# Performance work log

Measured on AMD Instinct MI355X. Metric: run time of the kernel, lower is better.

## Reference

```python
import jax, jax.numpy as jnp
import numpy as np


def conv2d(x, w, b, pad):
    # x: [B,Cin,H,W], w: [Cout,Cin,kh,kw]
    y = jax.lax.conv_general_dilated(
        x, w, window_strides=(1, 1), padding=[(pad, pad), (pad, pad)],
        dimension_numbers=('NCHW', 'OIHW', 'NCHW'))
    return y + b[None, :, None, None]


def setup_inputs() -> dict:
    key = jax.random.key(0)
    ks = jax.random.split(key, 11)
    B, C, H, W = 4, 128, 64, 64
    Cc, Hc, Wc = 256, 32, 32
    s = 0.05
    return {
        'sr_feat': jax.random.normal(ks[0], (B, C, H, W), jnp.float32),
        'context_feat': jax.random.normal(ks[1], (B, Cc, Hc, Wc), jnp.float32),
        'Wq': jax.random.normal(ks[2], (C, C, 1, 1), jnp.float32) * s,
        'bq': jax.random.normal(ks[3], (C,), jnp.float32) * s,
        'Wk': jax.random.normal(ks[4], (C, Cc, 1, 1), jnp.float32) * s,
        'bk': jax.random.normal(ks[5], (C,), jnp.float32) * s,
        'Wv': jax.random.normal(ks[6], (C, Cc, 1, 1), jnp.float32) * s,
        'bv': jax.random.normal(ks[7], (C,), jnp.float32) * s,
        'Wp': jax.random.normal(ks[8], (C, C, 3, 3), jnp.float32) * s,
        'bp': jax.random.normal(ks[9], (C,), jnp.float32) * s,
        'gamma': jax.random.normal(ks[10], (1,), jnp.float32) * s,
    }


def reference(sr_feat, context_feat, Wq, bq, Wk, bk, Wv, bv, Wp, bp, gamma):
    B, C, H, W = sr_feat.shape
    Cc = context_feat.shape[1]
    # bilinear upsample (half-pixel centers == align_corners=False)
    ctx = jax.image.resize(context_feat, (B, Cc, H, W), method='bilinear')
    q = conv2d(sr_feat, Wq, bq, 0).reshape(B, C, H * W)   # [B,C,N]
    k = conv2d(ctx, Wk, bk, 0).reshape(B, C, H * W)       # [B,C,N]
    v = conv2d(ctx, Wv, bv, 0).reshape(B, C, H * W)       # [B,C,N]
    # attn[b,n,m] = softmax_m( sum_c q[b,c,n] * k[b,c,m] )
    attn = jax.nn.softmax(jnp.einsum('bcn,bcm->bnm', q, k), axis=-1)
    # out[b,c,n] = sum_m v[b,c,m] * attn[b,n,m]
    out = jnp.einsum('bcm,bnm->bcn', v, attn).reshape(B, C, H, W)
    return sr_feat + gamma[0] * conv2d(out, Wp, bp, 1)
```

## Files before the change

kernel.cpp:

```cpp
#include <hip/hip_runtime.h>
#include <math.h>

#define NB 4
#define C  128
#define CCH 256
#define HH 64
#define WW 64
#define NN 4096
#define NS 1024
#define HC 32
#define WC 32
#define PP 66
#define LOG2E 1.44269504088896f
#define NSPLIT 4

typedef unsigned short u16;
typedef unsigned int uint32;
typedef short s16x8 __attribute__((ext_vector_type(8)));
typedef float f32x4 __attribute__((ext_vector_type(4)));
typedef float f32x16 __attribute__((ext_vector_type(16)));

#if __has_builtin(__builtin_amdgcn_exp2f)
#define EXP2(x) __builtin_amdgcn_exp2f(x)
#else
#define EXP2(x) __expf((x) * 0.69314718056f)
#endif

__device__ __forceinline__ u16 f2bf(float f) {
    uint32 u = __float_as_uint(f);
    u += 0x7fffu + ((u >> 16) & 1u);
    return (u16)(u >> 16);
}
__device__ __forceinline__ float bf2f(u16 h) {
    return __uint_as_float((uint32)h << 16);
}

__global__ __launch_bounds__(256) void prep2(const float* __restrict__ ctx,
                                             const float* __restrict__ sr,
                                             const float* __restrict__ Wq,
                                             const float* __restrict__ Wk,
                                             const float* __restrict__ Wv,
                                             const float* __restrict__ Wp,
                                             u16* __restrict__ ctx_s,
                                             u16* __restrict__ sr_t,
                                             u16* __restrict__ wbf,
                                             u16* __restrict__ wt,
                                             uint4* __restrict__ att_z) {
    __shared__ float ls[64 * 65];
    int blk = blockIdx.x;
    int tid = threadIdx.x;

    if (blk < 256) {
        int idx = blk;
        int n0 = (idx & 15) * 64;
        int ci0 = ((idx >> 4) & 3) * 64;
        int b = idx >> 6;
        const float* inb = ctx + ((size_t)b * CCH + ci0) * NS + n0;
#pragma unroll
        for (int L = 0; L < 4; L++) {
            int fc = tid + L * 256;
            int nc = fc & 15, ci = fc >> 4;
            float4 v = *(const float4*)(inb + (size_t)ci * NS + nc * 4);
            float* d = &ls[ci * 65 + nc * 4];
            d[0] = v.x; d[1] = v.y; d[2] = v.z; d[3] = v.w;
        }
        __syncthreads();
        u16* ob = ctx_s + ((size_t)b * NS + n0) * CCH + ci0;
#pragma unroll
        for (int j = 0; j < 16; j++) {
            int o = tid + j * 256;
            int ci = o & 63, n = o >> 6;
            ob[(size_t)n * CCH + ci] = f2bf(ls[ci * 65 + n]);
        }
    } else if (blk < 768) {
        int idx = blk - 256;
        int n0 = (idx & 63) * 64;
        int ci0 = ((idx >> 6) & 1) * 64;
        int b = idx >> 7;
        const float* inb = sr + ((size_t)b * C + ci0) * NN + n0;
#pragma unroll
        for (int L = 0; L < 4; L++) {
            int fc = tid + L * 256;
            int nc = fc & 15, ci = fc >> 4;
            float4 v = *(const float4*)(inb + (size_t)ci * NN + nc * 4);
            float* d = &ls[ci * 65 + nc * 4];
            d[0] = v.x; d[1] = v.y; d[2] = v.z; d[3] = v.w;
        }
        __syncthreads();
        u16* ob = sr_t + ((size_t)b * NN + n0) * C + ci0;
#pragma unroll
        for (int j = 0; j < 16; j++) {
            int o = tid + j * 256;
            int ci = o & 63, n = o >> 6;
            ob[(size_t)n * C + ci] = f2bf(ls[ci * 65 + n]);
        }
    } else if (blk < 1664) {
        int i = (blk - 768) * 256 + tid;
        if (i < 81920) {
            float v;
            if (i < 16384) v = Wq[i] * LOG2E;
            else if (i < 49152) v = Wk[i - 16384];
            else v = Wv[i - 49152];
            wbf[i] = f2bf(v);
        } else {
            int idx = i - 81920;
            int ciin = idx & 31;
            int co = (idx >> 5) & 127;
            int cb = (idx >> 12) & 3;
            int pos = idx >> 14;
            int ky = pos / 3, kx = pos - ky * 3;
            int ci = cb * 32 + ciin;
            wt[idx] = f2bf(Wp[((size_t)(co * C + ci) * 3 + ky) * 3 + kx]);
        }
    } else {
        int i = (blk - 1664) * 256 + tid;
        if (i < 278784) att_z[i] = make_uint4(0, 0, 0, 0);
    }
}

__global__ __launch_bounds__(256) void proj_all2(const u16* __restrict__ sr_t,
                                                 const u16* __restrict__ ctx_s,
                                                 const u16* __restrict__ wbf,
                                                 const float* __restrict__ bq,
                                                 const float* __restrict__ bk,
                                                 const float* __restrict__ bv,
                                                 u16* __restrict__ q_t,
                                                 u16* __restrict__ k_s,
                                                 u16* __restrict__ v_s) {
    __shared__ u16 xs[128 * 64];
    __shared__ u16 wsm[2][128 * 64];
    int b = blockIdx.y;
    int tid = threadIdx.x;
    int w = tid >> 6, lane = tid & 63, l31 = lane & 31, half = lane >> 5;
    int xh = w >> 1, wh = w & 1;

    if (blockIdx.x < 32) {
        int n0 = blockIdx.x * 128;
        const u16* xb = sr_t + (size_t)b * NN * C;
        f32x16 acc[2][2];
#pragma unroll
        for (int xt = 0; xt < 2; xt++)
#pragma unroll
            for (int wt2 = 0; wt2 < 2; wt2++)
#pragma unroll
                for (int i = 0; i < 16; i++) acc[xt][wt2][i] = 0.f;
        for (int c0i = 0; c0i < 2; c0i++) {
            int c0 = c0i * 64;
            __syncthreads();
#pragma unroll
            for (int t = 0; t < 4; t++) {
                int CI = t * 256 + tid;
                int row = CI >> 3, sl = CI & 7;
                int lc = sl ^ (row & 7);
                __builtin_amdgcn_global_load_lds(
                    (const __attribute__((address_space(1))) void*)(xb + (size_t)(n0 + row) * C + c0 + lc * 8),
                    (__attribute__((address_space(3))) void*)&xs[(size_t)CI * 8], 16, 0, 0);
            }
#pragma unroll
            for (int t = 0; t < 4; t++) {
                int CI = t * 256 + tid;
                int co = CI >> 3, sl = CI & 7;
                int lc = sl ^ (co & 7);
                __builtin_amdgcn_global_load_lds(
                    (const __attribute__((address_space(1))) void*)(wbf + (size_t)co * C + c0 + lc * 8),
                    (__attribute__((address_space(3))) void*)&wsm[0][(size_t)CI * 8], 16, 0, 0);
            }
            __syncthreads();
#pragma unroll
            for (int kg = 0; kg < 4; kg++) {
                int pc = ((kg * 2 + half) ^ (l31 & 7)) * 8;
                s16x8 xf[2], wf2[2];
#pragma unroll
                for (int xt = 0; xt < 2; xt++)
                    xf[xt] = *(const s16x8*)&xs[(xh * 64 + xt * 32 + l31) * 64 + pc];
#pragma unroll
                for (int wt2 = 0; wt2 < 2; wt2++)
                    wf2[wt2] = *(const s16x8*)&wsm[0][(wh * 64 + wt2 * 32 + l31) * 64 + pc];
#pragma unroll
                for (int xt = 0; xt < 2; xt++)
#pragma unroll
                    for (int wt2 = 0; wt2 < 2; wt2++)
                        acc[xt][wt2] = __builtin_amdgcn_mfma_f32_32x32x16_bf16(xf[xt], wf2[wt2], acc[xt][wt2], 0, 0, 0);
            }
        }
        u16* ot = q_t + (size_t)b * NN * C;
        float bv2[2];
#pragma unroll
        for (int wt2 = 0; wt2 < 2; wt2++) bv2[wt2] = bq[wh * 64 + wt2 * 32 + l31] * LOG2E;
#pragma unroll
        for (int xt = 0; xt < 2; xt++)
#pragma unroll
            for (int r = 0; r < 16; r++) {
                int n = n0 + xh * 64 + xt * 32 + (r & 3) + 8 * (r >> 2) + 4 * half;
#pragma unroll
                for (int wt2 = 0; wt2 < 2; wt2++)
                    ot[(size_t)n * C + wh * 64 + wt2 * 32 + l31] = f2bf(acc[xt][wt2][r] + bv2[wt2]);
            }
    } else {
        int n0 = (blockIdx.x - 32) * 64;
        const u16* xb = ctx_s + (size_t)b * NS * CCH;
        const u16* wkb = wbf + 16384;
        const u16* wvb = wbf + 49152;
        f32x16 acck[2], accv[2];
#pragma unroll
        for (int wt2 = 0; wt2 < 2; wt2++)
#pragma unroll
            for (int i = 0; i < 16; i++) { acck[wt2][i] = 0.f; accv[wt2][i] = 0.f; }
        for (int c0i = 0; c0i < 4; c0i++) {
            int c0 = c0i * 64;
            __syncthreads();
#pragma unroll
            for (int t = 0; t < 2; t++) {
                int CI = t * 256 + tid;
                int row = CI >> 3, sl = CI & 7;
                int lc = sl ^ (row & 7);
                __builtin_amdgcn_global_load_lds(
                    (const __attribute__((address_space(1))) void*)(xb + (size_t)(n0 + row) * CCH + c0 + lc * 8),
                    (__attribute__((address_space(3))) void*)&xs[(size_t)CI * 8], 16, 0, 0);
            }
#pragma unroll
            for (int t = 0; t < 4; t++) {
                int CI = t * 256 + tid;
                int co = CI >> 3, sl = CI & 7;
                int lc = sl ^ (co & 7);
                __builtin_amdgcn_global_load_lds(
                    (const __attribute__((address_space(1))) void*)(wkb + (size_t)co * CCH + c0 + lc * 8),
                    (__attribute__((address_space(3))) void*)&wsm[0][(size_t)CI * 8], 16, 0, 0);
            }
#pragma unroll
            for (int t = 0; t < 4; t++) {
                int CI = t * 256 + tid;
                int co = CI >> 3, sl = CI & 7;
                int lc = sl ^ (co & 7);
                __builtin_amdgcn_global_load_lds(
                    (const __attribute__((address_space(1))) void*)(wvb + (size_t)co * CCH + c0 + lc * 8),
                    (__attribute__((address_space(3))) void*)&wsm[1][(size_t)CI * 8], 16, 0, 0);
            }
            __syncthreads();
#pragma unroll
            for (int kg = 0; kg < 4; kg++) {
                int pc = ((kg * 2 + half) ^ (l31 & 7)) * 8;
                s16x8 xf = *(const s16x8*)&xs[(xh * 32 + l31) * 64 + pc];
                s16x8 wfk[2], wfv[2];
#pragma unroll
                for (int wt2 = 0; wt2 < 2; wt2++) {
                    wfk[wt2] = *(const s16x8*)&wsm[0][(wh * 64 + wt2 * 32 + l31) * 64 + pc];
                    wfv[wt2] = *(const s16x8*)&wsm[1][(wh * 64 + wt2 * 32 + l31) * 64 + pc];
                }
#pragma unroll
                for (int wt2 = 0; wt2 < 2; wt2++) {
                    acck[wt2] = __builtin_amdgcn_mfma_f32_32x32x16_bf16(xf, wfk[wt2], acck[wt2], 0, 0, 0);
                    accv[wt2] = __builtin_amdgcn_mfma_f32_32x32x16_bf16(wfv[wt2], xf, accv[wt2], 0, 0, 0);
                }
            }
        }
        u16* ok = k_s + (size_t)b * NS * C;
#pragma unroll
        for (int wt2 = 0; wt2 < 2; wt2++) {
            float bvk = bk[wh * 64 + wt2 * 32 + l31];
#pragma unroll
            for (int r = 0; r < 16; r++) {
                int n = n0 + xh * 32 + (r & 3) + 8 * (r >> 2) + 4 * half;
                ok[(size_t)n * C + wh * 64 + wt2 * 32 + l31] = f2bf(acck[wt2][r] + bvk);
            }
        }
        u16* ov = v_s + (size_t)b * C * NS;
#pragma unroll
        for (int wt2 = 0; wt2 < 2; wt2++)
#pragma unroll
            for (int r = 0; r < 16; r++) {
                int co = wh * 64 + wt2 * 32 + (r & 3) + 8 * (r >> 2) + 4 * half;
                ov[(size_t)co * NS + n0 + xh * 32 + l31] = f2bf(accv[wt2][r] + bv[co]);
            }
    }
}

__global__ __launch_bounds__(256) void upsample_v(const u16* __restrict__ v_s,
                                                  u16* __restrict__ v_bf) {
    __shared__ u16 lsv[NS];
    int idx = blockIdx.x;
    int tid = threadIdx.x;
    int c = idx & 127, b = idx >> 7;
    const u16* vp = v_s + ((size_t)b * C + c) * NS;
    if (tid < 128) *(uint4*)&lsv[tid * 8] = *(const uint4*)(vp + tid * 8);
    __syncthreads();
    u16* ob = v_bf + ((size_t)b * C + c) * NN;
#pragma unroll
    for (int j = 0; j < 16; j++) {
        int n = tid + j * 256;
        int y = n >> 6, x = n & 63;
        float sy = y * 0.5f - 0.25f;
        float sx = x * 0.5f - 0.25f;
        int y0 = (int)floorf(sy), x0 = (int)floorf(sx);
        float wy = sy - (float)y0, wx = sx - (float)x0;
        int y0c = y0 < 0 ? 0 : y0;
        int y1c = (y0 + 1 > HC - 1) ? HC - 1 : y0 + 1;
        int x0c = x0 < 0 ? 0 : x0;
        int x1c = (x0 + 1 > WC - 1) ? WC - 1 : x0 + 1;
        float v00 = bf2f(lsv[y0c * WC + x0c]), v01 = bf2f(lsv[y0c * WC + x1c]);
        float v10 = bf2f(lsv[y1c * WC + x0c]), v11 = bf2f(lsv[y1c * WC + x1c]);
        ob[n] = f2bf((1.f - wy) * ((1.f - wx) * v00 + wx * v01)
                   +        wy  * ((1.f - wx) * v10 + wx * v11));
    }
}

__global__ __launch_bounds__(256, 2) void flash_mfma(const u16* __restrict__ qt_p,
                                                     const u16* __restrict__ ks_p,
                                                     const u16* __restrict__ vt_p,
                                                     u16* __restrict__ part,
                                                     float* __restrict__ lpart) {
    __shared__ u16 ksr[3][32 * 128];
    __shared__ u16 vs[2][128 * 64];

    int ib = blockIdx.x;
    int b = (ib & 7) >> 1;
    int rest = ((ib >> 3) << 1) | (ib & 1);
    int qtile = rest >> 2;
    int split = rest & 3;
    int n0 = qtile * 128;
    int tid = threadIdx.x;
    int w = tid >> 6, lane = tid & 63, l31 = lane & 31, half = lane >> 5;

    const u16* qtb = qt_p + (size_t)b * NN * C;
    const u16* ksb = ks_p + (size_t)b * NS * C;
    const u16* vtb = vt_p + (size_t)b * C * NN;

    auto stageKrow = [&](int buf, int r) {
#pragma unroll
        for (int t = 0; t < 2; t++) {
            int CI = t * 256 + tid;
            int row = CI >> 4;
            int lc = (CI & 15) ^ (row & 15);
            __builtin_amdgcn_global_load_lds(
                (const __attribute__((address_space(1))) void*)(ksb + (size_t)(r * 32 + row) * C + lc * 8),
                (__attribute__((address_space(3))) void*)&ksr[buf][(size_t)CI * 8], 16, 0, 0);
        }
    };
    auto stageV = [&](int buf, int m0) {
#pragma unroll
        for (int t = 0; t < 4; t++) {
            int CI = (w * 4 + t) * 64 + lane;
            int c = CI >> 3;
            int lc = (CI & 7) ^ (c & 7);
            __builtin_amdgcn_global_load_lds(
                (const __attribute__((address_space(1))) void*)(vtb + (size_t)c * NN + m0 + lc * 8),
                (__attribute__((address_space(3))) void*)&vs[buf][(w * 4 + t) * 512], 16, 0, 0);
        }
    };

    int qrow = n0 + w * 32 + l31;
    s16x8 qf[8];
#pragma unroll
    for (int kg = 0; kg < 8; kg++)
        qf[kg] = *(const s16x8*)(qtb + (size_t)qrow * C + kg * 16 + half * 8);

    auto scoreTile = [&](int buf) {
        f32x16 st;
#pragma unroll
        for (int i = 0; i < 16; i++) st[i] = 0.f;
        const u16* kb = &ksr[buf][0];
#pragma unroll
        for (int kg = 0; kg < 8; kg++) {
            int pc = ((kg * 2 + half) ^ (l31 & 15)) * 8;
            s16x8 kf = *(const s16x8*)&kb[l31 * 128 + pc];
            st = __builtin_amdgcn_mfma_f32_32x32x16_bf16(kf, qf[kg], st, 0, 0, 0);
        }
        return st;
    };

    int m_base = split * 1024;
    int j0 = split * 8;

    stageKrow(0, split == 0 ? 0 : j0 - 1);
    stageKrow(1, j0);
    stageKrow(2, j0 + 1);
    stageV(0, m_base);
    __syncthreads();
    f32x16 sA = scoreTile(0);
    f32x16 sB = scoreTile(1);
    f32x16 sC;

    f32x16 oacc[4];
#pragma unroll
    for (int mt = 0; mt < 4; mt++)
#pragma unroll
        for (int i = 0; i < 16; i++) oacc[mt][i] = 0.f;
    float lsum = 0.f;

#pragma unroll 2
    for (int it = 0; it < 16; it++) {
        int buf = it & 1;
        int m0 = m_base + it * 64;
        if (it < 15) {
            stageV(buf ^ 1, m0 + 64);
            if (it & 1) {
                int rs = j0 + 2 + (it >> 1);
                if (rs <= 31) stageKrow((it >> 1) % 3, rs);
            }
        }
        if (!(it & 1)) {
            int rn = j0 + 1 + (it >> 1);
            if (rn <= 31) sC = scoreTile((2 + (it >> 1)) % 3);
        } else {
            sA = sB;
            int rn = j0 + 1 + (it >> 1);
            if (rn <= 31) sB = sC;
        }

        float wB = (it & 1) ? 0.25f : 0.75f;
        float wA = 1.0f - wB;
        float cc[16];
#pragma unroll
        for (int i = 0; i < 16; i++) cc[i] = wA * sA[i] + wB * sB[i];

        float xr0  = __shfl_xor(cc[0], 32);
        float xr3  = __shfl_xor(cc[3], 32);
        float xr4  = __shfl_xor(cc[4], 32);
        float xr7  = __shfl_xor(cc[7], 32);
        float xr8  = __shfl_xor(cc[8], 32);
        float xr11 = __shfl_xor(cc[11], 32);
        float xr12 = __shfl_xor(cc[12], 32);
        float xr15 = __shfl_xor(cc[15], 32);
        float d0s[4], d5s[4];
        d0s[0] = half ? xr3  : cc[0];
        d0s[1] = half ? xr7  : xr3;
        d0s[2] = half ? xr11 : xr7;
        d0s[3] = half ? xr15 : xr11;
        d5s[0] = half ? xr4  : xr0;
        d5s[1] = half ? xr8  : xr4;
        d5s[2] = half ? xr12 : xr8;
        d5s[3] = half ? cc[15] : xr12;

        const u16* vsb = &vs[buf][0];
#pragma unroll
        for (int s = 0; s < 4; s++) {
            float d0 = d0s[s], d1 = cc[4 * s], d2 = cc[4 * s + 1];
            float d3 = cc[4 * s + 2], d4 = cc[4 * s + 3], d5 = d5s[s];
            float e1 = 0.75f * d1, e2 = 0.75f * d2, e3 = 0.75f * d3, e4 = 0.75f * d4;
            float p0 = EXP2(fmaf(0.25f, d0, e1));
            float p1 = EXP2(fmaf(0.25f, d2, e1));
            float p2 = EXP2(fmaf(0.25f, d1, e2));
            float p3 = EXP2(fmaf(0.25f, d3, e2));
            float p4 = EXP2(fmaf(0.25f, d2, e3));
            float p5 = EXP2(fmaf(0.25f, d4, e3));
            float p6 = EXP2(fmaf(0.25f, d3, e4));
            float p7 = EXP2(fmaf(0.25f, d5, e4));
            lsum += ((p0 + p1) + (p2 + p3)) + ((p4 + p5) + (p6 + p7));
            union { uint32 u[4]; s16x8 v; } pu;
            pu.u[0] = __builtin_amdgcn_perm(__float_as_uint(p1), __float_as_uint(p0), 0x07060302u);
            pu.u[1] = __builtin_amdgcn_perm(__float_as_uint(p3), __float_as_uint(p2), 0x07060302u);
            pu.u[2] = __builtin_amdgcn_perm(__float_as_uint(p5), __float_as_uint(p4), 0x07060302u);
            pu.u[3] = __builtin_amdgcn_perm(__float_as_uint(p7), __float_as_uint(p6), 0x07060302u);
            int pcv = ((s * 2 + half) ^ (l31 & 7)) * 8;
#pragma unroll
            for (int mt = 0; mt < 4; mt++) {
                s16x8 vf = *(const s16x8*)&vsb[(mt * 32 + l31) * 64 + pcv];
                oacc[mt] = __builtin_amdgcn_mfma_f32_32x32x16_bf16(vf, pu.v, oacc[mt], 0, 0, 0);
            }
        }
        __syncthreads();
    }

    float lt = lsum + __shfl_xor(lsum, 32);
    if (half == 0) lpart[(size_t)split * NB * NN + (size_t)b * NN + qrow] = lt;
    u16* pb = part + ((size_t)split * NB + b) * (size_t)C * NN;
#pragma unroll
    for (int mt = 0; mt < 4; mt++)
#pragma unroll
        for (int r = 0; r < 16; r++) {
            int c = mt * 32 + (r & 3) + 8 * (r >> 2) + 4 * half;
            pb[(size_t)c * NN + n0 + w * 32 + l31] = f2bf(oacc[mt][r]);
        }
}

__global__ __launch_bounds__(256) void flash_combine(const u16* __restrict__ part,
                                                     const float* __restrict__ lpart,
                                                     u16* __restrict__ att_t) {
    __shared__ u16 ts[128 * 66];
    __shared__ float linv[64];
    int b = blockIdx.y;
    int nt = blockIdx.x;
    int n0 = nt * 64;
    int tid = threadIdx.x;
    if (tid < 64) {
        float s = 0.f;
#pragma unroll
        for (int sp = 0; sp < NSPLIT; sp++)
            s += lpart[(size_t)sp * NB * NN + (size_t)b * NN + n0 + tid];
        linv[tid] = 1.0f / s;
    }
    __syncthreads();
#pragma unroll
    for (int j = 0; j < 32; j++) {
        int e = tid + j * 256;
        int n = e & 63, c = e >> 6;
        float o = 0.f;
#pragma unroll
        for (int sp = 0; sp < NSPLIT; sp++)
            o += bf2f(part[((size_t)sp * NB + b) * (size_t)C * NN + (size_t)c * NN + n0 + n]);
        ts[c * 66 + n] = f2bf(o * linv[n]);
    }
    __syncthreads();
    u16* ob = att_t + ((size_t)b * PP * PP + (size_t)(nt + 1) * PP + 1) * C;
#pragma unroll
    for (int j = 0; j < 32; j++) {
        int o = tid + j * 256;
        int c = o & 127, n = o >> 7;
        ob[(size_t)n * C + c] = ts[c * 66 + n];
    }
}

__global__ __launch_bounds__(256) void conv3x3_mfma(const u16* __restrict__ att_t,
                                                    const u16* __restrict__ wt,
                                                    const float* __restrict__ bp,
                                                    const float* __restrict__ sr,
                                                    const float* __restrict__ gamma,
                                                    float* __restrict__ out) {
    __shared__ u16 in_s[2][4 * 102 * 8];
    int ib = blockIdx.x;
    int b = (ib & 7) >> 1;
    int rr = ((ib >> 3) << 1) | (ib & 1);
    int y = rr >> 1;
    int x0 = (rr & 1) * 32;
    int tid = threadIdx.x;
    int w = tid >> 6, lane = tid & 63, l = tid & 15, quad = (tid >> 4) & 3;
    const u16* ab = att_t + (size_t)b * (PP * PP * C);

    auto stage = [&](int cib, int bufi) {
        u16* base = &in_s[bufi][w * 102 * 8];
        const u16* gsrc = ab + cib * 32 + w * 8;
#pragma unroll
        for (int t = 0; t < 2; t++) {
            int idx = t * 64 + lane;
            int r = idx / 34, xp = idx - r * 34;
            if (t == 0 || lane < 38)
                __builtin_amdgcn_global_load_lds(
                    (const __attribute__((address_space(1))) void*)(gsrc + (size_t)((y + r) * PP + x0 + xp) * C),
                    (__attribute__((address_space(3))) void*)(base + (size_t)t * 64 * 8), 16, 0, 0);
        }
    };

    f32x4 accr[2][2];
#pragma unroll
    for (int cf = 0; cf < 2; cf++)
#pragma unroll
        for (int nf = 0; nf < 2; nf++) accr[cf][nf] = (f32x4){0.f, 0.f, 0.f, 0.f};
    int cow = w * 32;

    stage(0, 0);
    __syncthreads();
#pragma unroll
    for (int cib = 0; cib < 4; cib++) {
        if (cib < 3) stage(cib + 1, (cib + 1) & 1);
        s16x8 wf[9][2];
#pragma unroll
        for (int pos = 0; pos < 9; pos++)
#pragma unroll
            for (int cf = 0; cf < 2; cf++)
                wf[pos][cf] = *(const s16x8*)&wt[((size_t)(pos * 4 + cib) * C + cow + cf * 16 + l) * 32 + quad * 8];
        const u16* bufc = &in_s[cib & 1][0];
#pragma unroll
        for (int ky = 0; ky < 3; ky++)
#pragma unroll
            for (int kx = 0; kx < 3; kx++) {
                int pos = ky * 3 + kx;
#pragma unroll
                for (int nf = 0; nf < 2; nf++) {
                    s16x8 inf = *(const s16x8*)&bufc[(quad * 102 + ky * 34 + nf * 16 + l + kx) * 8];
                    accr[0][nf] = __builtin_amdgcn_mfma_f32_16x16x32_bf16(wf[pos][0], inf, accr[0][nf], 0, 0, 0);
                    accr[1][nf] = __builtin_amdgcn_mfma_f32_16x16x32_bf16(wf[pos][1], inf, accr[1][nf], 0, 0, 0);
                }
            }
        __syncthreads();
    }

    float g = gamma[0];
    float* ob = out + (size_t)b * C * NN;
    const float* sb = sr + (size_t)b * C * NN;
#pragma unroll
    for (int cf = 0; cf < 2; cf++)
#pragma unroll
        for (int r = 0; r < 4; r++) {
            int co = cow + cf * 16 + quad * 4 + r;
            float bias = bp[co];
#pragma unroll
            for (int nf = 0; nf < 2; nf++) {
                size_t oo = (size_t)co * NN + y * 64 + x0 + nf * 16 + l;
                ob[oo] = sb[oo] + g * (accr[cf][nf][r] + bias);
            }
        }
}

extern "C" void kernel_launch(void* const* d_in, const int* in_sizes, int n_in,
                              void* d_out, int out_size, void* d_ws, size_t ws_size,
                              hipStream_t stream) {
    const float* sr    = (const float*)d_in[0];
    const float* ctx   = (const float*)d_in[1];
    const float* Wq    = (const float*)d_in[2];
    const float* bq    = (const float*)d_in[3];
    const float* Wk    = (const float*)d_in[4];
    const float* bk    = (const float*)d_in[5];
    const float* Wv    = (const float*)d_in[6];
    const float* bv    = (const float*)d_in[7];
    const float* Wp    = (const float*)d_in[8];
    const float* bp    = (const float*)d_in[9];
    const float* gamma = (const float*)d_in[10];
    float* out = (float*)d_out;

    char* wsb = (char*)d_ws;
    u16*   att_t  = (u16*)wsb;
    u16*   part   = (u16*)(wsb + (5u << 20));
    float* lpart  = (float*)(wsb + (21u << 20));
    u16*   ctx_s  = (u16*)(wsb + (22u << 20));
    u16*   sr_t   = (u16*)(wsb + (25u << 20));
    u16*   q_t    = (u16*)(wsb + (29u << 20));
    u16*   k_s    = (u16*)(wsb + (33u << 20));
    u16*   v_s    = (u16*)(wsb + (34u << 20));
    u16*   v_bf   = (u16*)(wsb + (39u << 20));
    u16*   wt     = (u16*)(wsb + (43u << 20));
    u16*   w_bf   = (u16*)(wsb + (43u << 20) + (512u << 10));

    prep2<<<dim3(2753), 256, 0, stream>>>(ctx, sr, Wq, Wk, Wv, Wp,
                                          ctx_s, sr_t, w_bf, wt, (uint4*)att_t);
    proj_all2<<<dim3(48, NB), 256, 0, stream>>>(sr_t, ctx_s, w_bf, bq, bk, bv,
                                                q_t, k_s, v_s);
    upsample_v<<<dim3(512), 256, 0, stream>>>(v_s, v_bf);
    flash_mfma<<<dim3(512), 256, 0, stream>>>(q_t, k_s, v_bf, part, lpart);
    flash_combine<<<dim3(64, NB), 256, 0, stream>>>(part, lpart, att_t);
    conv3x3_mfma<<<dim3(512), 256, 0, stream>>>(att_t, wt, bp, sr, gamma, out);
}
```

Baseline: 150.2 us.

## Fold V upsampling into attention weights and drop upsample_v kernel

Bilinear upsampling is linear, so attention against the upsampled V equals attention against low-resolution V with the probability rows folded by the transposed interpolation weights. The flash kernel now accumulates the folded probabilities per coarse row into two rotating accumulators and runs P·V against the 32x32 V directly. This removes the upsample_v launch, the full-resolution V buffer and its LDS staging, and cuts the P·V MFMA work. In exchange V fragments are read straight from global memory without LDS, there is extra VALU and shuffle work to fold the probabilities, and the edge-weight handling at split boundaries is subtle.

```diff
diff --git a/kernel.cpp b/kernel.cpp
--- a/kernel.cpp
+++ b/kernel.cpp
@@ -275,42 +275,12 @@
     }
 }
 
-__global__ __launch_bounds__(256) void upsample_v(const u16* __restrict__ v_s,
-                                                  u16* __restrict__ v_bf) {
-    __shared__ u16 lsv[NS];
-    int idx = blockIdx.x;
-    int tid = threadIdx.x;
-    int c = idx & 127, b = idx >> 7;
-    const u16* vp = v_s + ((size_t)b * C + c) * NS;
-    if (tid < 128) *(uint4*)&lsv[tid * 8] = *(const uint4*)(vp + tid * 8);
-    __syncthreads();
-    u16* ob = v_bf + ((size_t)b * C + c) * NN;
-#pragma unroll
-    for (int j = 0; j < 16; j++) {
-        int n = tid + j * 256;
-        int y = n >> 6, x = n & 63;
-        float sy = y * 0.5f - 0.25f;
-        float sx = x * 0.5f - 0.25f;
-        int y0 = (int)floorf(sy), x0 = (int)floorf(sx);
-        float wy = sy - (float)y0, wx = sx - (float)x0;
-        int y0c = y0 < 0 ? 0 : y0;
-        int y1c = (y0 + 1 > HC - 1) ? HC - 1 : y0 + 1;
-        int x0c = x0 < 0 ? 0 : x0;
-        int x1c = (x0 + 1 > WC - 1) ? WC - 1 : x0 + 1;
-        float v00 = bf2f(lsv[y0c * WC + x0c]), v01 = bf2f(lsv[y0c * WC + x1c]);
-        float v10 = bf2f(lsv[y1c * WC + x0c]), v11 = bf2f(lsv[y1c * WC + x1c]);
-        ob[n] = f2bf((1.f - wy) * ((1.f - wx) * v00 + wx * v01)
-                   +        wy  * ((1.f - wx) * v10 + wx * v11));
-    }
-}
-
 __global__ __launch_bounds__(256, 2) void flash_mfma(const u16* __restrict__ qt_p,
                                                      const u16* __restrict__ ks_p,
-                                                     const u16* __restrict__ vt_p,
+                                                     const u16* __restrict__ vs_p,
                                                      u16* __restrict__ part,
                                                      float* __restrict__ lpart) {
     __shared__ u16 ksr[3][32 * 128];
-    __shared__ u16 vs[2][128 * 64];
 
     int ib = blockIdx.x;
     int b = (ib & 7) >> 1;
@@ -323,7 +293,7 @@
 
     const u16* qtb = qt_p + (size_t)b * NN * C;
     const u16* ksb = ks_p + (size_t)b * NS * C;
-    const u16* vtb = vt_p + (size_t)b * C * NN;
+    const u16* vtb = vs_p + (size_t)b * C * NS;
 
     auto stageKrow = [&](int buf, int r) {
 #pragma unroll
@@ -336,17 +306,6 @@
                 (__attribute__((address_space(3))) void*)&ksr[buf][(size_t)CI * 8], 16, 0, 0);
         }
     };
-    auto stageV = [&](int buf, int m0) {
-#pragma unroll
-        for (int t = 0; t < 4; t++) {
-            int CI = (w * 4 + t) * 64 + lane;
-            int c = CI >> 3;
-            int lc = (CI & 7) ^ (c & 7);
-            __builtin_amdgcn_global_load_lds(
-                (const __attribute__((address_space(1))) void*)(vtb + (size_t)c * NN + m0 + lc * 8),
-                (__attribute__((address_space(3))) void*)&vs[buf][(w * 4 + t) * 512], 16, 0, 0);
-        }
-    };
 
     int qrow = n0 + w * 32 + l31;
     s16x8 qf[8];
@@ -368,13 +327,11 @@
         return st;
     };
 
-    int m_base = split * 1024;
     int j0 = split * 8;
 
     stageKrow(0, split == 0 ? 0 : j0 - 1);
     stageKrow(1, j0);
     stageKrow(2, j0 + 1);
-    stageV(0, m_base);
     __syncthreads();
     f32x16 sA = scoreTile(0);
     f32x16 sB = scoreTile(1);
@@ -385,34 +342,45 @@
     for (int mt = 0; mt < 4; mt++)
 #pragma unroll
         for (int i = 0; i < 16; i++) oacc[mt][i] = 0.f;
+    f32x16 acc0, acc1;
+#pragma unroll
+    for (int i = 0; i < 16; i++) { acc0[i] = 0.f; acc1[i] = 0.f; }
     float lsum = 0.f;
 
-#pragma unroll 2
-    for (int it = 0; it < 16; it++) {
-        int buf = it & 1;
-        int m0 = m_base + it * 64;
-        if (it < 15) {
-            stageV(buf ^ 1, m0 + 64);
-            if (it & 1) {
-                int rs = j0 + 2 + (it >> 1);
-                if (rs <= 31) stageKrow((it >> 1) % 3, rs);
-            }
-        }
-        if (!(it & 1)) {
-            int rn = j0 + 1 + (it >> 1);
-            if (rn <= 31) sC = scoreTile((2 + (it >> 1)) % 3);
-        } else {
-            sA = sB;
-            int rn = j0 + 1 + (it >> 1);
-            if (rn <= 31) sB = sC;
-        }
-
-        float wB = (it & 1) ? 0.25f : 0.75f;
-        float wA = 1.0f - wB;
-        float cc[16];
+    auto doPV = [&](int r, f32x16& ac) {
+        uint32 own[8], rcv[8];
+#pragma unroll
+        for (int s = 0; s < 4; s++) {
+            own[2 * s]     = __builtin_amdgcn_perm(__float_as_uint(ac[4 * s + 1]), __float_as_uint(ac[4 * s + 0]), 0x07060302u);
+            own[2 * s + 1] = __builtin_amdgcn_perm(__float_as_uint(ac[4 * s + 3]), __float_as_uint(ac[4 * s + 2]), 0x07060302u);
+        }
+#pragma unroll
+        for (int i = 0; i < 8; i++) rcv[i] = __shfl_xor(own[i], 32);
+        union { uint32 u[4]; s16x8 v; } pf0, pf1;
+        pf0.u[0] = half ? rcv[2] : own[0];
+        pf0.u[1] = half ? rcv[3] : own[1];
+        pf0.u[2] = half ? own[2] : rcv[0];
+        pf0.u[3] = half ? own[3] : rcv[1];
+        pf1.u[0] = half ? rcv[6] : own[4];
+        pf1.u[1] = half ? rcv[7] : own[5];
+        pf1.u[2] = half ? own[6] : rcv[4];
+        pf1.u[3] = half ? own[7] : rcv[5];
+        const u16* vr = vtb + (size_t)l31 * NS + (size_t)r * 32 + half * 8;
+#pragma unroll
+        for (int mt = 0; mt < 4; mt++) {
+            s16x8 vf0 = *(const s16x8*)(vr + (size_t)mt * 32 * NS);
+            s16x8 vf1 = *(const s16x8*)(vr + (size_t)mt * 32 * NS + 16);
+            oacc[mt] = __builtin_amdgcn_mfma_f32_32x32x16_bf16(vf0, pf0.v, oacc[mt], 0, 0, 0);
+            oacc[mt] = __builtin_amdgcn_mfma_f32_32x32x16_bf16(vf1, pf1.v, oacc[mt], 0, 0, 0);
+        }
+#pragma unroll
+        for (int i = 0; i < 16; i++) ac[i] = 0.f;
+    };
+
+    auto process = [&](float wA, float wB, float wlo, float whi, f32x16& alo, f32x16& ahi) {
+        f32x16 cc;
 #pragma unroll
         for (int i = 0; i < 16; i++) cc[i] = wA * sA[i] + wB * sB[i];
-
         float xr0  = __shfl_xor(cc[0], 32);
         float xr3  = __shfl_xor(cc[3], 32);
         float xr4  = __shfl_xor(cc[4], 32);
@@ -431,35 +399,85 @@
         d5s[2] = half ? xr12 : xr8;
         d5s[3] = half ? cc[15] : xr12;
 
-        const u16* vsb = &vs[buf][0];
+        float ps[4][8];
+        float r0a[4], r7a[4];
 #pragma unroll
         for (int s = 0; s < 4; s++) {
             float d0 = d0s[s], d1 = cc[4 * s], d2 = cc[4 * s + 1];
             float d3 = cc[4 * s + 2], d4 = cc[4 * s + 3], d5 = d5s[s];
             float e1 = 0.75f * d1, e2 = 0.75f * d2, e3 = 0.75f * d3, e4 = 0.75f * d4;
-            float p0 = EXP2(fmaf(0.25f, d0, e1));
-            float p1 = EXP2(fmaf(0.25f, d2, e1));
-            float p2 = EXP2(fmaf(0.25f, d1, e2));
-            float p3 = EXP2(fmaf(0.25f, d3, e2));
-            float p4 = EXP2(fmaf(0.25f, d2, e3));
-            float p5 = EXP2(fmaf(0.25f, d4, e3));
-            float p6 = EXP2(fmaf(0.25f, d3, e4));
-            float p7 = EXP2(fmaf(0.25f, d5, e4));
-            lsum += ((p0 + p1) + (p2 + p3)) + ((p4 + p5) + (p6 + p7));
-            union { uint32 u[4]; s16x8 v; } pu;
-            pu.u[0] = __builtin_amdgcn_perm(__float_as_uint(p1), __float_as_uint(p0), 0x07060302u);
-            pu.u[1] = __builtin_amdgcn_perm(__float_as_uint(p3), __float_as_uint(p2), 0x07060302u);
-            pu.u[2] = __builtin_amdgcn_perm(__float_as_uint(p5), __float_as_uint(p4), 0x07060302u);
-            pu.u[3] = __builtin_amdgcn_perm(__float_as_uint(p7), __float_as_uint(p6), 0x07060302u);
-            int pcv = ((s * 2 + half) ^ (l31 & 7)) * 8;
-#pragma unroll
-            for (int mt = 0; mt < 4; mt++) {
-                s16x8 vf = *(const s16x8*)&vsb[(mt * 32 + l31) * 64 + pcv];
-                oacc[mt] = __builtin_amdgcn_mfma_f32_32x32x16_bf16(vf, pu.v, oacc[mt], 0, 0, 0);
-            }
-        }
-        __syncthreads();
+            ps[s][0] = EXP2(fmaf(0.25f, d0, e1));
+            ps[s][1] = EXP2(fmaf(0.25f, d2, e1));
+            ps[s][2] = EXP2(fmaf(0.25f, d1, e2));
+            ps[s][3] = EXP2(fmaf(0.25f, d3, e2));
+            ps[s][4] = EXP2(fmaf(0.25f, d2, e3));
+            ps[s][5] = EXP2(fmaf(0.25f, d4, e3));
+            ps[s][6] = EXP2(fmaf(0.25f, d3, e4));
+            ps[s][7] = EXP2(fmaf(0.25f, d5, e4));
+            r0a[s] = __shfl_xor(ps[s][0], 32);
+            r7a[s] = __shfl_xor(ps[s][7], 32);
+        }
+        float tq[16];
+#pragma unroll
+        for (int s = 0; s < 4; s++) {
+            float pl = half ? r7a[s] : (s ? r7a[s - 1] : ps[0][0]);
+            float pr = half ? (s < 3 ? r0a[s + 1] : ps[3][7]) : r0a[s];
+            tq[4 * s + 0] = fmaf(0.25f, pl,       fmaf(0.75f, ps[s][0], fmaf(0.75f, ps[s][1], 0.25f * ps[s][2])));
+            tq[4 * s + 1] = fmaf(0.25f, ps[s][1], fmaf(0.75f, ps[s][2], fmaf(0.75f, ps[s][3], 0.25f * ps[s][4])));
+            tq[4 * s + 2] = fmaf(0.25f, ps[s][3], fmaf(0.75f, ps[s][4], fmaf(0.75f, ps[s][5], 0.25f * ps[s][6])));
+            tq[4 * s + 3] = fmaf(0.25f, ps[s][5], fmaf(0.75f, ps[s][6], fmaf(0.75f, ps[s][7], 0.25f * pr)));
+        }
+        float l0 = ((tq[0] + tq[1]) + (tq[2] + tq[3])) + ((tq[4] + tq[5]) + (tq[6] + tq[7]));
+        float l1 = ((tq[8] + tq[9]) + (tq[10] + tq[11])) + ((tq[12] + tq[13]) + (tq[14] + tq[15]));
+        lsum += l0 + l1;
+#pragma unroll
+        for (int i = 0; i < 16; i++) {
+            alo[i] = fmaf(wlo, tq[i], alo[i]);
+            ahi[i] = fmaf(whi, tq[i], ahi[i]);
+        }
+    };
+
+    float w0lo = (split == 0) ? 0.f : 0.25f;
+    float w0hi = (split == 0) ? 1.f : 0.75f;
+    float w15lo = (split == 3) ? 1.f : 0.75f;
+    float w15hi = (split == 3) ? 0.f : 0.25f;
+
+#pragma unroll
+    for (int it = 0; it < 16; it++) {
+        if ((it & 1) == 0) {
+            int rn = j0 + 1 + (it >> 1);
+            if (rn <= 31) sC = scoreTile((2 + (it >> 1)) % 3);
+            float wlo = (it == 0) ? w0lo : 0.25f;
+            float whi = (it == 0) ? w0hi : 0.75f;
+            f32x16& alo = (((it >> 1) & 1) == 0) ? acc0 : acc1;
+            f32x16& ahi = (((it >> 1) & 1) == 0) ? acc1 : acc0;
+            process(0.25f, 0.75f, wlo, whi, alo, ahi);
+            if (it != 0) {
+                doPV(j0 + (it >> 1) - 1, alo);
+            } else if (split != 0) {
+                doPV(j0 - 1, alo);
+            }
+            if (it == 0) __syncthreads();
+        } else {
+            if (it < 15) {
+                int rs = j0 + 2 + (it >> 1);
+                if (rs <= 31) stageKrow((it >> 1) % 3, rs);
+            }
+            sA = sB;
+            {
+                int rn = j0 + 1 + (it >> 1);
+                if (rn <= 31) sB = sC;
+            }
+            float wlo = (it == 15) ? w15lo : 0.75f;
+            float whi = (it == 15) ? w15hi : 0.25f;
+            f32x16& alo = ((((it >> 1) + 1) & 1) == 0) ? acc0 : acc1;
+            f32x16& ahi = ((((it >> 1) + 1) & 1) == 0) ? acc1 : acc0;
+            process(0.75f, 0.25f, wlo, whi, alo, ahi);
+            if (it < 15) __syncthreads();
+        }
     }
+    doPV(j0 + 7, acc0);
+    if (split < 3) doPV(j0 + 8, acc1);
 
     float lt = lsum + __shfl_xor(lsum, 32);
     if (half == 0) lpart[(size_t)split * NB * NN + (size_t)b * NN + qrow] = lt;
@@ -616,7 +634,6 @@
     u16*   q_t    = (u16*)(wsb + (29u << 20));
     u16*   k_s    = (u16*)(wsb + (33u << 20));
     u16*   v_s    = (u16*)(wsb + (34u << 20));
-    u16*   v_bf   = (u16*)(wsb + (39u << 20));
     u16*   wt     = (u16*)(wsb + (43u << 20));
     u16*   w_bf   = (u16*)(wsb + (43u << 20) + (512u << 10));
 
@@ -624,8 +641,7 @@
                                           ctx_s, sr_t, w_bf, wt, (uint4*)att_t);
     proj_all2<<<dim3(48, NB), 256, 0, stream>>>(sr_t, ctx_s, w_bf, bq, bk, bv,
                                                 q_t, k_s, v_s);
-    upsample_v<<<dim3(512), 256, 0, stream>>>(v_s, v_bf);
-    flash_mfma<<<dim3(512), 256, 0, stream>>>(q_t, k_s, v_bf, part, lpart);
+    flash_mfma<<<dim3(512), 256, 0, stream>>>(q_t, k_s, v_s, part, lpart);
     flash_combine<<<dim3(64, NB), 256, 0, stream>>>(part, lpart, att_t);
     conv3x3_mfma<<<dim3(512), 256, 0, stream>>>(att_t, wt, bp, sr, gamma, out);
 }
```

Result: slower. 211.6 us (+40.8%).
